# Kernel optimization log

Hardware: AMD Instinct MI355X
Metric: run time of the kernel (lower is better)

## Reference

```python
import jax, jax.numpy as jnp
import numpy as np

SEQ, BATCH = 512, 128
FEAT_CH, EMBED = 1024, 1024
N_LANG = 8  # tgt_lang_toks = [0..7]


def setup_inputs() -> dict:
    key = jax.random.key(0)
    k_feat, k_tok, k_w, k_b = jax.random.split(key, 4)
    feat = jax.random.normal(k_feat, (SEQ, BATCH, FEAT_CH), dtype=jnp.float32)
    tgt_lang_toks = jax.random.randint(k_tok, (BATCH,), 0, N_LANG, dtype=jnp.int64)
    # stacked per-language Linear params: W[l] is [embed, feat] (torch Linear layout), b[l] is [embed]
    bound = 1.0 / np.sqrt(FEAT_CH)
    W = jax.random.uniform(k_w, (N_LANG, EMBED, FEAT_CH), minval=-bound, maxval=bound, dtype=jnp.float32)
    b = jax.random.uniform(k_b, (N_LANG, EMBED), minval=-bound, maxval=bound, dtype=jnp.float32)
    return {"feat": feat, "W": W, "b": b, "tgt_lang_toks": tgt_lang_toks}


def reference(feat, W, b, tgt_lang_toks):
    # Each batch column uses the Linear of its language token. Since the
    # language token values equal their index in tgt_lang_toks=[0..7], the
    # per-group mask/gather/scatter of the original collapses to a per-batch
    # weight gather + batched matmul (grouped GEMM as dense dispatch).
    toks = tgt_lang_toks.astype(jnp.int32)
    W_sel = W[toks]          # [B, E, F]
    b_sel = b[toks]          # [B, E]
    # [S,B,F] x [B,E,F] -> [S,B,E]
    out = jnp.einsum('sbf,bef->sbe', feat, W_sel) + b_sel[None, :, :]
    return out
```

## Files before the change

### kernel.cpp

```cpp
#include <hip/hip_runtime.h>
#include <hip/hip_bf16.h>

#define SEQ   512
#define BATCH 128
#define FEAT  1024
#define EMBED 1024
#define NLANG 8

typedef __attribute__((ext_vector_type(8))) short bf16x8;
typedef __attribute__((ext_vector_type(4))) float f32x4;
typedef unsigned short ushort_t;

__device__ __forceinline__ unsigned pk2(float a, float b) {
  float2 f; f.x = a; f.y = b;
  __hip_bfloat162 h = __float22bfloat162_rn(f);
  union { __hip_bfloat162 h2; unsigned u; } cv;
  cv.h2 = h;
  return cv.u;
}

__device__ __forceinline__ void gld16(const void* g, void* l) {
  __builtin_amdgcn_global_load_lds(
      (const __attribute__((address_space(1))) void*)g,
      (__attribute__((address_space(3))) void*)l, 16, 0, 0);
}

__global__ __launch_bounds__(256) void convert_permute_kernel(
    const float* __restrict__ feat,
    const float* __restrict__ Wf,
    const int*   __restrict__ toks,
    ushort_t* __restrict__ Abf,
    ushort_t* __restrict__ Wbf)
{
  __shared__ int stok[128];
  __shared__ int srank[128];
  __shared__ int scnt[8];
  __shared__ int sbase[8];

  const int tid = threadIdx.x;
  if (tid < 128) stok[tid] = toks[tid];
  __syncthreads();
  if (tid < 128) {
    int myt = stok[tid], r = 0;
    for (int j = 0; j < 128; ++j) r += (j < tid) && (stok[j] == myt);
    srank[tid] = r;
  }
  if (tid < 8) {
    int c = 0;
    for (int j = 0; j < 128; ++j) c += (stok[j] == tid);
    scnt[tid] = c;
  }
  __syncthreads();
  if (tid < 8) {
    int b = 0;
    for (int j = 0; j < tid; ++j) b += scnt[j];
    sbase[tid] = b << 9;
  }
  __syncthreads();

  const int FC = (SEQ * BATCH * FEAT) / 4;
  const int TC = FC + (NLANG * EMBED * FEAT) / 4;
  for (int c = blockIdx.x * 256 + tid; c < TC; c += gridDim.x * 256) {
    if (c < FC) {
      float4 v = ((const float4*)feat)[c];
      const int r = c >> 8, q = c & 255;
      const int b = r & 127, s = r >> 7;
      const int tk = stok[b];
      const int p = sbase[tk] + s * scnt[tk] + srank[b];
      uint2 o; o.x = pk2(v.x, v.y); o.y = pk2(v.z, v.w);
      *(uint2*)(Abf + ((size_t)p << 10) + (q << 2)) = o;
    } else {
      const int c2 = c - FC;
      float4 v = ((const float4*)Wf)[c2];
      uint2 o; o.x = pk2(v.x, v.y); o.y = pk2(v.z, v.w);
      *(uint2*)(Wbf + ((size_t)c2 << 2)) = o;
    }
  }
}

__global__ __launch_bounds__(512, 2) void grouped_gemm_8ph(
    const ushort_t* __restrict__ Abf,
    const ushort_t* __restrict__ Wbf,
    const float* __restrict__ bias,
    const int*   __restrict__ toks,
    float*       __restrict__ out)
{
  extern __shared__ ushort_t lds[];
  __shared__ int tokarr[128];
  __shared__ unsigned long long ballots[2][8];
  __shared__ int perm[128];
  __shared__ int rowsrc[256];

  const int tid = threadIdx.x;
  const int l   = tid & 63;
  const int w   = tid >> 6;
  const int wr  = w >> 2;
  const int wc  = w & 3;

  const int bid = blockIdx.x;
  const int L   = (bid & 7) * 128 + (bid >> 3);
  const int et  = L & 3;
  const int mt  = (L >> 7) * 32 + ((L >> 2) & 31);
  const int m0  = mt * 256;
  const int e0  = et * 256;

  if (tid < 128) tokarr[tid] = toks[tid];
  __syncthreads();
  if (tid < 128) {
    int myt = tokarr[tid];
#pragma unroll
    for (int lg = 0; lg < 8; ++lg) {
      unsigned long long bl = __ballot(myt == lg);
      if (l == 0) ballots[w][lg] = bl;
    }
  }
  __syncthreads();

  int lsel = 0, base = 0, csel = 1, boff_sel = 0;
  {
    int cum = 0, boff = 0;
#pragma unroll
    for (int lg = 0; lg < 8; ++lg) {
      int c = __popcll(ballots[0][lg]) + __popcll(ballots[1][lg]);
      int seg = c << 9;
      bool in = (m0 >= cum) && (m0 < cum + seg);
      if (in) { lsel = lg; base = cum; csel = c; boff_sel = boff; }
      cum += seg; boff += c;
    }
  }

  if (tid < 128) {
    int myt = tokarr[tid];
    unsigned long long ltm = (1ull << l) - 1ull;
    int rank = (w == 0) ? __popcll(ballots[0][myt] & ltm)
                        : __popcll(ballots[0][myt]) + __popcll(ballots[1][myt] & ltm);
    int boff2 = 0;
#pragma unroll
    for (int lg = 0; lg < 8; ++lg) {
      int c = __popcll(ballots[0][lg]) + __popcll(ballots[1][lg]);
      boff2 += (lg < myt) ? c : 0;
    }
    perm[boff2 + rank] = tid;
  }
  __syncthreads();
  if (tid < 256) {
    int local = m0 - base + tid;
    int s = local / csel;
    int j = local - s * csel;
    rowsrc[tid] = s * BATCH + perm[boff_sel + j];
  }
  __syncthreads();

  const int ca   = w * 128 + l;
  const int rwA  = ca >> 2;
  const int ccA  = ca & 3;
  const int sA   = (rwA >> 1) & 3;
  const ushort_t* aS0 = Abf + (size_t)(m0 + rwA) * FEAT + ((ccA ^ sA) * 8);
  const ushort_t* aS1 = aS0 + (size_t)16 * FEAT;
  const ushort_t* bS0 = Wbf + ((size_t)lsel * EMBED + e0 + rwA) * FEAT + ((ccA ^ sA) * 8);
  const ushort_t* bS1 = bS0 + (size_t)16 * FEAT;
  const int dOff0 = (w * 128) * 8;
  const int dOff1 = (w * 128 + 64) * 8;

  const int kc  = l >> 4;
  const int rA  = wr * 128 + (l & 15);
  const int aRd = rA * 32 + ((kc ^ ((rA >> 1) & 3)) * 8);
  const int rB  = wc * 64 + (l & 15);
  const int bRd = rB * 32 + ((kc ^ ((rB >> 1) & 3)) * 8);

  f32x4 acc[8][4] = {};
  bf16x8 af0[4], af1[4], bfq[4];

#define STAGE_A(kt, buf)                                                   \
  do { const int _o = (kt) * 32;                                           \
    gld16(aS0 + _o, lds + (buf) * 8192 + dOff0);                           \
    gld16(aS1 + _o, lds + (buf) * 8192 + dOff1); } while (0)
#define STAGE_B(kt, buf)                                                   \
  do { const int _o = (kt) * 32;                                           \
    gld16(bS0 + _o, lds + 32768 + (buf) * 8192 + dOff0);                   \
    gld16(bS1 + _o, lds + 32768 + (buf) * 8192 + dOff1); } while (0)

#define PH0(g, DOSTAGE)                                                    \
  do {                                                                     \
    const ushort_t* Ab_ = lds + ((g) & 3) * 8192;                          \
    const ushort_t* Bb_ = lds + 32768 + ((g) & 3) * 8192;                  \
    _Pragma("unroll") for (int mf = 0; mf < 4; ++mf)                       \
        af0[mf] = *(const bf16x8*)(Ab_ + aRd + mf * 512);                  \
    _Pragma("unroll") for (int nf = 0; nf < 4; ++nf)                       \
        bfq[nf] = *(const bf16x8*)(Bb_ + bRd + nf * 512);                  \
    if (DOSTAGE) { STAGE_A((g) + 3, ((g) + 3) & 3); }                      \
    __builtin_amdgcn_sched_barrier(0);                                     \
    __builtin_amdgcn_s_barrier();                                          \
    asm volatile("s_waitcnt lgkmcnt(0)" ::: "memory");                     \
    __builtin_amdgcn_sched_barrier(0);                                     \
    __builtin_amdgcn_s_setprio(1);                                         \
    _Pragma("unroll") for (int mf = 0; mf < 4; ++mf)                       \
        _Pragma("unroll") for (int nf = 0; nf < 4; ++nf)                   \
            acc[mf][nf] = __builtin_amdgcn_mfma_f32_16x16x32_bf16(         \
                af0[mf], bfq[nf], acc[mf][nf], 0, 0, 0);                   \
    __builtin_amdgcn_s_setprio(0);                                         \
    __builtin_amdgcn_s_barrier();                                          \
  } while (0)

#define PH1(g, DOSTAGE, WAIT)                                              \
  do {                                                                     \
    const ushort_t* Ab_ = lds + ((g) & 3) * 8192;                          \
    _Pragma("unroll") for (int mf = 0; mf < 4; ++mf)                       \
        af1[mf] = *(const bf16x8*)(Ab_ + aRd + (mf + 4) * 512);            \
    if (DOSTAGE) { STAGE_B((g) + 3, ((g) + 3) & 3); }                      \
    __builtin_amdgcn_sched_barrier(0);                                     \
    __builtin_amdgcn_s_barrier();                                          \
    asm volatile("s_waitcnt lgkmcnt(0)" ::: "memory");                     \
    __builtin_amdgcn_sched_barrier(0);                                     \
    __builtin_amdgcn_s_setprio(1);                                         \
    _Pragma("unroll") for (int mf = 0; mf < 4; ++mf)                       \
        _Pragma("unroll") for (int nf = 0; nf < 4; ++nf)                   \
            acc[mf + 4][nf] = __builtin_amdgcn_mfma_f32_16x16x32_bf16(     \
                af1[mf], bfq[nf], acc[mf + 4][nf], 0, 0, 0);               \
    __builtin_amdgcn_s_setprio(0);                                         \
    asm volatile(WAIT ::: "memory");                                       \
    __builtin_amdgcn_s_barrier();                                          \
  } while (0)

  STAGE_A(0, 0); STAGE_B(0, 0);
  STAGE_A(1, 1); STAGE_B(1, 1);
  STAGE_A(2, 2); STAGE_B(2, 2);
  asm volatile("s_waitcnt vmcnt(8)" ::: "memory");
  __builtin_amdgcn_s_barrier();
  __builtin_amdgcn_sched_barrier(0);

  for (int g = 0; g < 29; ++g) {
    PH0(g, true);
    PH1(g, true, "s_waitcnt vmcnt(8)");
  }
  PH0(29, false); PH1(29, false, "s_waitcnt vmcnt(4)");
  PH0(30, false); PH1(30, false, "s_waitcnt vmcnt(0)");
  PH0(31, false); PH1(31, false, "s_nop 0");

#undef PH0
#undef PH1
#undef STAGE_A
#undef STAGE_B

  const int col = l & 15;
  const int r4  = (l >> 4) * 4;
  float bvv[4];
#pragma unroll
  for (int nf = 0; nf < 4; ++nf)
    bvv[nf] = bias[lsel * EMBED + e0 + wc * 64 + nf * 16 + col];
#pragma unroll
  for (int mf = 0; mf < 8; ++mf) {
#pragma unroll
    for (int j = 0; j < 4; ++j) {
      const size_t ro = (size_t)rowsrc[wr * 128 + mf * 16 + r4 + j] * EMBED;
#pragma unroll
      for (int nf = 0; nf < 4; ++nf)
        out[ro + e0 + wc * 64 + nf * 16 + col] = acc[mf][nf][j] + bvv[nf];
    }
  }
}

__global__ __launch_bounds__(256, 2) void grouped_proj_fused(
    const float* __restrict__ feat, const float* __restrict__ Wt,
    const float* __restrict__ bias, const int* __restrict__ toks,
    float* __restrict__ out)
{
  __shared__ uint4 As[1024];
  __shared__ uint4 Bs[1024];
  __shared__ int tokarr[128];
  __shared__ unsigned long long ballots[2][8];
  __shared__ int perm[128];
  __shared__ int rowsrc[128];

  const int tid  = threadIdx.x;
  const int lane = tid & 63;
  const int wv   = tid >> 6;
  const int wr   = wv >> 1;
  const int wc   = wv & 1;
  const int bid = blockIdx.x;
  const int xcd = bid & 7;
  const int sq  = bid >> 3;
  const int et  = sq & 7;
  const int mt  = (sq >> 3) * 8 + xcd;
  const int m0  = mt * 128;
  const int e0  = et * 128;

  if (tid < 128) tokarr[tid] = toks[tid];
  __syncthreads();
  if (tid < 128) {
    int myt = tokarr[tid];
#pragma unroll
    for (int lg = 0; lg < 8; ++lg) {
      unsigned long long bl = __ballot(myt == lg);
      if (lane == 0) ballots[wv][lg] = bl;
    }
  }
  __syncthreads();
  int lsel = 0, base = 0, csel = 1, boff_sel = 0;
  {
    int cum = 0, boff = 0;
#pragma unroll
    for (int lg = 0; lg < 8; ++lg) {
      int c = __popcll(ballots[0][lg]) + __popcll(ballots[1][lg]);
      int seg = c << 9;
      bool in = (m0 >= cum) && (m0 < cum + seg);
      if (in) { lsel = lg; base = cum; csel = c; boff_sel = boff; }
      cum += seg; boff += c;
    }
  }
  if (tid < 128) {
    int myt = tokarr[tid];
    unsigned long long ltm = (1ull << lane) - 1ull;
    int rank = (wv == 0) ? __popcll(ballots[0][myt] & ltm)
                         : __popcll(ballots[0][myt]) + __popcll(ballots[1][myt] & ltm);
    int boff2 = 0;
#pragma unroll
    for (int lg = 0; lg < 8; ++lg) {
      int c = __popcll(ballots[0][lg]) + __popcll(ballots[1][lg]);
      boff2 += (lg < myt) ? c : 0;
    }
    perm[boff2 + rank] = tid;
  }
  __syncthreads();
  if (tid < 128) {
    int local = m0 - base + tid;
    int s = local / csel;
    int j = local - s * csel;
    rowsrc[tid] = s * BATCH + perm[boff_sel + j];
  }
  __syncthreads();

  int slot_i[4];
  const float* aptr[4];
  const float* bptr[4];
#pragma unroll
  for (int it = 0; it < 4; ++it) {
    int c    = it * 256 + tid;
    int kg   = c & 7;
    int row  = c >> 3;
    int ksub = kg & 3;
    int kk   = kg >> 2;
    int frag = row >> 4;
    slot_i[it] = (kk * 8 + frag) * 64 + ((row & 15) ^ (ksub << 1) ^ kk) + ksub * 16;
    aptr[it] = feat + (size_t)rowsrc[row] * FEAT + kg * 8;
    bptr[it] = Wt + ((size_t)lsel * EMBED + e0 + row) * FEAT + kg * 8;
  }

  f32x4 acc[4][4] = {};
  for (int k0 = 0; k0 < FEAT; k0 += 64) {
    __syncthreads();
#pragma unroll
    for (int it = 0; it < 4; ++it) {
      float4 alo = *(const float4*)(aptr[it] + k0);
      float4 ahi = *(const float4*)(aptr[it] + k0 + 4);
      uint4 av;
      av.x = pk2(alo.x, alo.y); av.y = pk2(alo.z, alo.w);
      av.z = pk2(ahi.x, ahi.y); av.w = pk2(ahi.z, ahi.w);
      As[slot_i[it]] = av;
      float4 blo = *(const float4*)(bptr[it] + k0);
      float4 bhi = *(const float4*)(bptr[it] + k0 + 4);
      uint4 bv;
      bv.x = pk2(blo.x, blo.y); bv.y = pk2(blo.z, blo.w);
      bv.z = pk2(bhi.x, bhi.y); bv.w = pk2(bhi.z, bhi.w);
      Bs[slot_i[it]] = bv;
    }
    __syncthreads();
#pragma unroll
    for (int kk = 0; kk < 2; ++kk) {
      const int ksr = lane >> 4;
      const int sw  = ((lane & 15) ^ (ksr << 1) ^ kk) + ksr * 16;
      bf16x8 af[4], bfr[4];
#pragma unroll
      for (int mi = 0; mi < 4; ++mi)
        af[mi] = ((const bf16x8*)As)[(kk * 8 + wr * 4 + mi) * 64 + sw];
#pragma unroll
      for (int ni = 0; ni < 4; ++ni)
        bfr[ni] = ((const bf16x8*)Bs)[(kk * 8 + wc * 4 + ni) * 64 + sw];
#pragma unroll
      for (int mi = 0; mi < 4; ++mi)
#pragma unroll
        for (int ni = 0; ni < 4; ++ni)
          acc[mi][ni] = __builtin_amdgcn_mfma_f32_16x16x32_bf16(
              af[mi], bfr[ni], acc[mi][ni], 0, 0, 0);
    }
  }

  const int col = lane & 15;
  const int r0  = (lane >> 4) * 4;
  float bvv[4];
#pragma unroll
  for (int ni = 0; ni < 4; ++ni)
    bvv[ni] = bias[lsel * EMBED + e0 + wc * 64 + ni * 16 + col];
#pragma unroll
  for (int mi = 0; mi < 4; ++mi) {
#pragma unroll
    for (int j = 0; j < 4; ++j) {
      const size_t ro = (size_t)rowsrc[wr * 64 + mi * 16 + r0 + j] * EMBED;
#pragma unroll
      for (int ni = 0; ni < 4; ++ni)
        out[ro + e0 + wc * 64 + ni * 16 + col] = acc[mi][ni][j] + bvv[ni];
    }
  }
}

extern "C" void kernel_launch(void* const* d_in, const int* in_sizes, int n_in,
                              void* d_out, int out_size, void* d_ws, size_t ws_size,
                              hipStream_t stream) {
  const float* feat = (const float*)d_in[0];
  const float* W    = (const float*)d_in[1];
  const float* bias = (const float*)d_in[2];
  const int*   toks = (const int*)d_in[3];
  float* out = (float*)d_out;

  const size_t abf_bytes = (size_t)SEQ * BATCH * FEAT * 2;
  const size_t wbf_bytes = (size_t)NLANG * EMBED * FEAT * 2;

  if (ws_size >= abf_bytes + wbf_bytes) {
    ushort_t* Abf = (ushort_t*)d_ws;
    ushort_t* Wbf = (ushort_t*)((char*)d_ws + abf_bytes);
    convert_permute_kernel<<<3072, 256, 0, stream>>>(feat, W, toks, Abf, Wbf);
    (void)hipFuncSetAttribute((const void*)grouped_gemm_8ph,
                              hipFuncAttributeMaxDynamicSharedMemorySize, 131072);
    const int nblk = (SEQ * BATCH / 256) * (EMBED / 256);
    grouped_gemm_8ph<<<nblk, 512, 131072, stream>>>(Abf, Wbf, bias, toks, out);
  } else {
    grouped_proj_fused<<<(SEQ * BATCH / 128) * (EMBED / 128), 256, 0, stream>>>(
        feat, W, bias, toks, out);
  }
}
```

Measured before the change: 260.7 us.

## Fuse feat gather and bf16 conversion into grouped GEMM A-tile loads

Drops the separate pass that converted and permuted all of feat into a bf16 workspace. The GEMM now gathers fp32 feat rows straight into LDS through per-row source indices and converts them to bf16 in registers just before the MFMAs. Only W is still pre-converted, by a smaller kernel. This removes a full-tensor write and re-read of the activation copy. In exchange it doubles the A-tile bytes per load and in LDS, cuts the LDS pipeline from three stages to two, adds conversion ALU work to the inner loop, and makes A loads scattered by row.

```diff
diff --git a/kernel.cpp b/kernel.cpp
--- a/kernel.cpp
+++ b/kernel.cpp
@@ -19,73 +19,40 @@
   return cv.u;
 }
 
+__device__ __forceinline__ bf16x8 cvt8(f32x4 lo, f32x4 hi) {
+  union { bf16x8 v; unsigned u[4]; } q;
+  q.u[0] = pk2(lo[0], lo[1]); q.u[1] = pk2(lo[2], lo[3]);
+  q.u[2] = pk2(hi[0], hi[1]); q.u[3] = pk2(hi[2], hi[3]);
+  return q.v;
+}
+
 __device__ __forceinline__ void gld16(const void* g, void* l) {
   __builtin_amdgcn_global_load_lds(
       (const __attribute__((address_space(1))) void*)g,
       (__attribute__((address_space(3))) void*)l, 16, 0, 0);
 }
 
-__global__ __launch_bounds__(256) void convert_permute_kernel(
+__global__ __launch_bounds__(256) void convert_w_kernel(
+    const float* __restrict__ Wf, ushort_t* __restrict__ Wbf)
+{
+  const int n = (NLANG * EMBED * FEAT) / 4;
+  for (int c = blockIdx.x * 256 + threadIdx.x; c < n; c += gridDim.x * 256) {
+    float4 v = ((const float4*)Wf)[c];
+    uint2 o; o.x = pk2(v.x, v.y); o.y = pk2(v.z, v.w);
+    *(uint2*)(Wbf + ((size_t)c << 2)) = o;
+  }
+}
+
+__global__ __launch_bounds__(512, 2) void grouped_gemm_fused(
     const float* __restrict__ feat,
-    const float* __restrict__ Wf,
-    const int*   __restrict__ toks,
-    ushort_t* __restrict__ Abf,
-    ushort_t* __restrict__ Wbf)
-{
-  __shared__ int stok[128];
-  __shared__ int srank[128];
-  __shared__ int scnt[8];
-  __shared__ int sbase[8];
-
-  const int tid = threadIdx.x;
-  if (tid < 128) stok[tid] = toks[tid];
-  __syncthreads();
-  if (tid < 128) {
-    int myt = stok[tid], r = 0;
-    for (int j = 0; j < 128; ++j) r += (j < tid) && (stok[j] == myt);
-    srank[tid] = r;
-  }
-  if (tid < 8) {
-    int c = 0;
-    for (int j = 0; j < 128; ++j) c += (stok[j] == tid);
-    scnt[tid] = c;
-  }
-  __syncthreads();
-  if (tid < 8) {
-    int b = 0;
-    for (int j = 0; j < tid; ++j) b += scnt[j];
-    sbase[tid] = b << 9;
-  }
-  __syncthreads();
-
-  const int FC = (SEQ * BATCH * FEAT) / 4;
-  const int TC = FC + (NLANG * EMBED * FEAT) / 4;
-  for (int c = blockIdx.x * 256 + tid; c < TC; c += gridDim.x * 256) {
-    if (c < FC) {
-      float4 v = ((const float4*)feat)[c];
-      const int r = c >> 8, q = c & 255;
-      const int b = r & 127, s = r >> 7;
-      const int tk = stok[b];
-      const int p = sbase[tk] + s * scnt[tk] + srank[b];
-      uint2 o; o.x = pk2(v.x, v.y); o.y = pk2(v.z, v.w);
-      *(uint2*)(Abf + ((size_t)p << 10) + (q << 2)) = o;
-    } else {
-      const int c2 = c - FC;
-      float4 v = ((const float4*)Wf)[c2];
-      uint2 o; o.x = pk2(v.x, v.y); o.y = pk2(v.z, v.w);
-      *(uint2*)(Wbf + ((size_t)c2 << 2)) = o;
-    }
-  }
-}
-
-__global__ __launch_bounds__(512, 2) void grouped_gemm_8ph(
-    const ushort_t* __restrict__ Abf,
     const ushort_t* __restrict__ Wbf,
     const float* __restrict__ bias,
     const int*   __restrict__ toks,
     float*       __restrict__ out)
 {
-  extern __shared__ ushort_t lds[];
+  extern __shared__ char ldsraw[];
+  float*    Af = (float*)ldsraw;
+  ushort_t* Bf = (ushort_t*)(ldsraw + 98304);
   __shared__ int tokarr[128];
   __shared__ unsigned long long ballots[2][8];
   __shared__ int perm[128];
@@ -151,20 +118,32 @@
   }
   __syncthreads();
 
-  const int ca   = w * 128 + l;
-  const int rwA  = ca >> 2;
-  const int ccA  = ca & 3;
-  const int sA   = (rwA >> 1) & 3;
-  const ushort_t* aS0 = Abf + (size_t)(m0 + rwA) * FEAT + ((ccA ^ sA) * 8);
-  const ushort_t* aS1 = aS0 + (size_t)16 * FEAT;
-  const ushort_t* bS0 = Wbf + ((size_t)lsel * EMBED + e0 + rwA) * FEAT + ((ccA ^ sA) * 8);
+  const float* aSrc[4];
+#pragma unroll
+  for (int i = 0; i < 4; ++i) {
+    const int c    = (w * 4 + i) * 64 + l;
+    const int row  = c >> 3;
+    const int slot = c & 7;
+    aSrc[i] = feat + (size_t)rowsrc[row] * FEAT + ((slot ^ (row & 7)) << 2);
+  }
+  const int aD0 = w * 1024;
+  const int aD1 = aD0 + 256;
+  const int aD2 = aD0 + 512;
+  const int aD3 = aD0 + 768;
+
+  const int ca  = w * 128 + l;
+  const int rwB = ca >> 2;
+  const int ccB = ca & 3;
+  const int sB  = (rwB >> 1) & 3;
+  const ushort_t* bS0 = Wbf + ((size_t)lsel * EMBED + e0 + rwB) * FEAT + ((ccB ^ sB) * 8);
   const ushort_t* bS1 = bS0 + (size_t)16 * FEAT;
-  const int dOff0 = (w * 128) * 8;
-  const int dOff1 = (w * 128 + 64) * 8;
-
-  const int kc  = l >> 4;
-  const int rA  = wr * 128 + (l & 15);
-  const int aRd = rA * 32 + ((kc ^ ((rA >> 1) & 3)) * 8);
+  const int bD0 = (w * 128) * 8;
+  const int bD1 = (w * 128 + 64) * 8;
+
+  const int kc    = l >> 4;
+  const int baseA = (wr * 128 + (l & 15)) * 32;
+  const int sl0   = ((2 * kc) ^ (l & 7)) * 4;
+  const int sl1   = ((2 * kc + 1) ^ (l & 7)) * 4;
   const int rB  = wc * 64 + (l & 15);
   const int bRd = rB * 32 + ((kc ^ ((rB >> 1) & 3)) * 8);
 
@@ -173,22 +152,27 @@
 
 #define STAGE_A(kt, buf)                                                   \
   do { const int _o = (kt) * 32;                                           \
-    gld16(aS0 + _o, lds + (buf) * 8192 + dOff0);                           \
-    gld16(aS1 + _o, lds + (buf) * 8192 + dOff1); } while (0)
+    gld16(aSrc[0] + _o, Af + (buf) * 8192 + aD0);                          \
+    gld16(aSrc[1] + _o, Af + (buf) * 8192 + aD1);                          \
+    gld16(aSrc[2] + _o, Af + (buf) * 8192 + aD2);                          \
+    gld16(aSrc[3] + _o, Af + (buf) * 8192 + aD3); } while (0)
 #define STAGE_B(kt, buf)                                                   \
   do { const int _o = (kt) * 32;                                           \
-    gld16(bS0 + _o, lds + 32768 + (buf) * 8192 + dOff0);                   \
-    gld16(bS1 + _o, lds + 32768 + (buf) * 8192 + dOff1); } while (0)
-
-#define PH0(g, DOSTAGE)                                                    \
+    gld16(bS0 + _o, Bf + (buf) * 8192 + bD0);                              \
+    gld16(bS1 + _o, Bf + (buf) * 8192 + bD1); } while (0)
+
+#define PH0(g, rbuf, sbuf, DOSTAGE)                                        \
   do {                                                                     \
-    const ushort_t* Ab_ = lds + ((g) & 3) * 8192;                          \
-    const ushort_t* Bb_ = lds + 32768 + ((g) & 3) * 8192;                  \
-    _Pragma("unroll") for (int mf = 0; mf < 4; ++mf)                       \
-        af0[mf] = *(const bf16x8*)(Ab_ + aRd + mf * 512);                  \
+    const float*    Ab_ = Af + (rbuf) * 8192;                              \
+    const ushort_t* Bb_ = Bf + (rbuf) * 8192;                              \
+    _Pragma("unroll") for (int mf = 0; mf < 4; ++mf) {                     \
+      f32x4 lo_ = *(const f32x4*)(Ab_ + baseA + mf * 512 + sl0);           \
+      f32x4 hi_ = *(const f32x4*)(Ab_ + baseA + mf * 512 + sl1);           \
+      af0[mf] = cvt8(lo_, hi_);                                            \
+    }                                                                      \
     _Pragma("unroll") for (int nf = 0; nf < 4; ++nf)                       \
-        bfq[nf] = *(const bf16x8*)(Bb_ + bRd + nf * 512);                  \
-    if (DOSTAGE) { STAGE_A((g) + 3, ((g) + 3) & 3); }                      \
+      bfq[nf] = *(const bf16x8*)(Bb_ + bRd + nf * 512);                    \
+    if (DOSTAGE) { STAGE_A((g) + 2, sbuf); }                               \
     __builtin_amdgcn_sched_barrier(0);                                     \
     __builtin_amdgcn_s_barrier();                                          \
     asm volatile("s_waitcnt lgkmcnt(0)" ::: "memory");                     \
@@ -202,12 +186,15 @@
     __builtin_amdgcn_s_barrier();                                          \
   } while (0)
 
-#define PH1(g, DOSTAGE, WAIT)                                              \
+#define PH1(g, rbuf, sbuf, DOSTAGE, WAIT)                                  \
   do {                                                                     \
-    const ushort_t* Ab_ = lds + ((g) & 3) * 8192;                          \
-    _Pragma("unroll") for (int mf = 0; mf < 4; ++mf)                       \
-        af1[mf] = *(const bf16x8*)(Ab_ + aRd + (mf + 4) * 512);            \
-    if (DOSTAGE) { STAGE_B((g) + 3, ((g) + 3) & 3); }                      \
+    const float* Ab_ = Af + (rbuf) * 8192;                                 \
+    _Pragma("unroll") for (int mf = 0; mf < 4; ++mf) {                     \
+      f32x4 lo_ = *(const f32x4*)(Ab_ + baseA + (mf + 4) * 512 + sl0);     \
+      f32x4 hi_ = *(const f32x4*)(Ab_ + baseA + (mf + 4) * 512 + sl1);     \
+      af1[mf] = cvt8(lo_, hi_);                                            \
+    }                                                                      \
+    if (DOSTAGE) { STAGE_B((g) + 2, sbuf); }                               \
     __builtin_amdgcn_sched_barrier(0);                                     \
     __builtin_amdgcn_s_barrier();                                          \
     asm volatile("s_waitcnt lgkmcnt(0)" ::: "memory");                     \
@@ -224,18 +211,19 @@
 
   STAGE_A(0, 0); STAGE_B(0, 0);
   STAGE_A(1, 1); STAGE_B(1, 1);
-  STAGE_A(2, 2); STAGE_B(2, 2);
-  asm volatile("s_waitcnt vmcnt(8)" ::: "memory");
+  asm volatile("s_waitcnt vmcnt(6)" ::: "memory");
   __builtin_amdgcn_s_barrier();
   __builtin_amdgcn_sched_barrier(0);
 
-  for (int g = 0; g < 29; ++g) {
-    PH0(g, true);
-    PH1(g, true, "s_waitcnt vmcnt(8)");
-  }
-  PH0(29, false); PH1(29, false, "s_waitcnt vmcnt(4)");
-  PH0(30, false); PH1(30, false, "s_waitcnt vmcnt(0)");
-  PH0(31, false); PH1(31, false, "s_nop 0");
+#pragma unroll 1
+  for (int gg = 0; gg < 10; ++gg) {
+    const int g = gg * 3;
+    PH0(g + 0, 0, 2, true);  PH1(g + 0, 0, 2, true, "s_waitcnt vmcnt(6)");
+    PH0(g + 1, 1, 0, true);  PH1(g + 1, 1, 0, true, "s_waitcnt vmcnt(6)");
+    PH0(g + 2, 2, 1, true);  PH1(g + 2, 2, 1, true, "s_waitcnt vmcnt(6)");
+  }
+  PH0(30, 0, 0, false); PH1(30, 0, 0, false, "s_waitcnt vmcnt(0)");
+  PH0(31, 1, 0, false); PH1(31, 1, 0, false, "s_nop 0");
 
 #undef PH0
 #undef PH1
@@ -412,17 +400,15 @@
   const int*   toks = (const int*)d_in[3];
   float* out = (float*)d_out;
 
-  const size_t abf_bytes = (size_t)SEQ * BATCH * FEAT * 2;
   const size_t wbf_bytes = (size_t)NLANG * EMBED * FEAT * 2;
 
-  if (ws_size >= abf_bytes + wbf_bytes) {
-    ushort_t* Abf = (ushort_t*)d_ws;
-    ushort_t* Wbf = (ushort_t*)((char*)d_ws + abf_bytes);
-    convert_permute_kernel<<<3072, 256, 0, stream>>>(feat, W, toks, Abf, Wbf);
-    (void)hipFuncSetAttribute((const void*)grouped_gemm_8ph,
-                              hipFuncAttributeMaxDynamicSharedMemorySize, 131072);
+  if (ws_size >= wbf_bytes) {
+    ushort_t* Wbf = (ushort_t*)d_ws;
+    convert_w_kernel<<<512, 256, 0, stream>>>(W, Wbf);
+    (void)hipFuncSetAttribute((const void*)grouped_gemm_fused,
+                              hipFuncAttributeMaxDynamicSharedMemorySize, 147456);
     const int nblk = (SEQ * BATCH / 256) * (EMBED / 256);
-    grouped_gemm_8ph<<<nblk, 512, 131072, stream>>>(Abf, Wbf, bias, toks, out);
+    grouped_gemm_fused<<<nblk, 512, 147456, stream>>>(feat, Wbf, bias, toks, out);
   } else {
     grouped_proj_fused<<<(SEQ * BATCH / 128) * (EMBED / 128), 256, 0, stream>>>(
         feat, W, bias, toks, out);
```

Result: faster. 241.5 us (-7.4%).
